# Optimization experiments

Hardware: AMD Instinct MI355X
Metric: run time of the kernel (lower is better)

## Reference

```python
import math
import jax, jax.numpy as jnp
import numpy as np

B, V, F, H, W = 1, 2, 4, 16, 28
TPF = H * W            # 448 tokens per frame
VS = F * TPF           # 1792 tokens per view
TS = V * VS            # 3584 total tokens
DIM, NH = 1536, 12
HD = DIM // NH         # 128
EPS = 1e-6
SCALE = 1.0 / math.sqrt(HD)


def _rope_angle_table(max_len=1024):
    # Wan-style 3D rope: head_dim//2 = 64 channels split [22, 21, 21] for (f, h, w)
    parts = []
    for full in (44, 42, 42):
        inv = 1.0 / (10000.0 ** (np.arange(0, full, 2) / full))
        parts.append(np.outer(np.arange(max_len), inv))
    return np.concatenate(parts, axis=1).astype(np.float32)  # [max_len, 64]


def setup_inputs():
    key = jax.random.key(0)
    ks = jax.random.split(key, 6)
    p = lambda k, shp: 0.02 * jax.random.normal(k, shp, dtype=jnp.float32)
    return {
        "x": jax.random.normal(ks[0], (B, TS, DIM), dtype=jnp.float32),
        "freqs": jnp.asarray(_rope_angle_table()),
        "q_w": p(ks[1], (DIM, DIM)), "q_b": jnp.zeros((DIM,), jnp.float32),
        "k_w": p(ks[2], (DIM, DIM)), "k_b": jnp.zeros((DIM,), jnp.float32),
        "v_w": p(ks[3], (DIM, DIM)), "v_b": jnp.zeros((DIM,), jnp.float32),
        "o_w": p(ks[4], (DIM, DIM)), "o_b": jnp.zeros((DIM,), jnp.float32),
        "norm_q_w": jnp.ones((DIM,), jnp.float32),
        "norm_k_w": jnp.ones((DIM,), jnp.float32),
        "seq_lens": jnp.full((B,), TS, jnp.int32),
        "view_grid_sizes": jnp.broadcast_to(jnp.array([F, H, W], jnp.int32), (B, V, 3)),
        "view_seq_lens": jnp.full((B, V), VS, jnp.int32),
        "total_seq_lens": jnp.full((B,), TS, jnp.int32),
    }


def _rms_norm(x, w):
    x32 = x.astype(jnp.float32)
    y = x32 * jax.lax.rsqrt(jnp.mean(x32 * x32, axis=-1, keepdims=True) + EPS)
    return y.astype(x.dtype) * w


def _rope_angles(freqs):
    c = HD // 2                                   # 64
    s0, s1 = c - 2 * (c // 3), c // 3             # 22, 21
    af = jnp.broadcast_to(freqs[:F, None, None, :s0], (F, H, W, s0))
    ah = jnp.broadcast_to(freqs[None, :H, None, s0:s0 + s1], (F, H, W, s1))
    aw = jnp.broadcast_to(freqs[None, None, :W, s0 + s1:c], (F, H, W, c - s0 - s1))
    return jnp.concatenate([af, ah, aw], axis=-1).reshape(VS, c)  # [VS, 64]


def _apply_rope(x, ang):
    # x: [N, S, NH, HD]; pairs are (x[..., 2i], x[..., 2i+1]) as in view_as_complex
    cos = jnp.cos(ang)[None, :, None, :]
    sin = jnp.sin(ang)[None, :, None, :]
    xr = x.reshape(x.shape[:-1] + (HD // 2, 2))
    r0 = xr[..., 0] * cos - xr[..., 1] * sin
    r1 = xr[..., 0] * sin + xr[..., 1] * cos
    return jnp.stack([r0, r1], axis=-1).reshape(x.shape)


def _attn_lse(q, k, v):
    # q,k,v: [N, S, NH, HD] -> out [N, S, NH, HD], lse [N, S, NH]
    logits = jnp.einsum('bqhd,bkhd->bhqk', q, k) * SCALE
    lse = jax.nn.logsumexp(logits, axis=-1)       # [N, NH, Sq]
    p = jnp.exp(logits - lse[..., None])
    out = jnp.einsum('bhqk,bkhd->bqhd', p, v)
    return out, jnp.transpose(lse, (0, 2, 1))


def _forward(x, freqs, q_w, q_b, k_w, k_b, v_w, v_b, o_w, o_b, norm_q_w, norm_k_w):
    xv = x[:, :TS]
    q = _rms_norm(xv @ q_w.T + q_b, norm_q_w)
    k = _rms_norm(xv @ k_w.T + k_b, norm_k_w)
    v = xv @ v_w.T + v_b
    q = q.reshape(B * V, VS, NH, HD)
    k = k.reshape(B * V, VS, NH, HD)
    v = v.reshape(B * V, VS, NH, HD)
    ang = _rope_angles(freqs)
    q = _apply_rope(q, ang)
    k = _apply_rope(k, ang)
    # intra-view attention over the full view sequence
    out_i, lse_i = _attn_lse(q, k, v)
    # cross-view per-frame attention: swap the two views for K/V
    k_sw = k.reshape(B, V, F, TPF, NH, HD)[:, ::-1].reshape(B * V * F, TPF, NH, HD)
    v_sw = v.reshape(B, V, F, TPF, NH, HD)[:, ::-1].reshape(B * V * F, TPF, NH, HD)
    q_c = q.reshape(B * V * F, TPF, NH, HD)
    out_c, lse_c = _attn_lse(q_c, k_sw, v_sw)
    out_i = out_i.reshape(B, V, F, TPF, NH, HD)
    lse_i = lse_i.reshape(B, V, F, TPF, NH)
    out_c = out_c.reshape(B, V, F, TPF, NH, HD)
    lse_c = lse_c.reshape(B, V, F, TPF, NH)
    # online-softmax-style LSE merge of the two attention results
    lse_u = jnp.logaddexp(lse_i, lse_c)
    fused = (jnp.exp(lse_i - lse_u)[..., None] * out_i
             + jnp.exp(lse_c - lse_u)[..., None] * out_c)
    fused = fused.reshape(B, TS, DIM)
    return fused @ o_w.T + o_b


def reference(x, freqs, q_w, q_b, k_w, k_b, v_w, v_b, o_w, o_b, norm_q_w, norm_k_w,
              seq_lens, view_grid_sizes, view_seq_lens, total_seq_lens):
    del seq_lens, view_grid_sizes, view_seq_lens, total_seq_lens  # validated layout constants
    return _forward(x, freqs, q_w, q_b, k_w, k_b, v_w, v_b, o_w, o_b, norm_q_w, norm_k_w)
```

## Files before the change

kernel.cpp:

```cpp
#include <hip/hip_runtime.h>

#define TS 3584
#define VS 1792
#define TPF 448
#define NHEAD 12
#define HDIM 128
#define DMODEL 1536
#define QK_PRESCALE (0.08838834764831845f * 1.4426950408889634f)

typedef unsigned short u16;
typedef unsigned int u32;
typedef __attribute__((ext_vector_type(8))) short bf16x8;
typedef __attribute__((ext_vector_type(4))) float f32x4;

__device__ __forceinline__ float u2f(u32 u) { union { u32 u; float f; } c; c.u = u; return c.f; }
__device__ __forceinline__ float blo(u32 u) { return u2f(u << 16); }
__device__ __forceinline__ float bhi(u32 u) { return u2f(u & 0xffff0000u); }
__device__ __forceinline__ u16 f2b(float f) {
  union { float f; u32 u; } c; c.f = f;
  return (u16)((c.u + 0x7fffu + ((c.u >> 16) & 1u)) >> 16);
}

__device__ __forceinline__ void gl16(const u16* g, u16* l) {
  __builtin_amdgcn_global_load_lds(
      (const __attribute__((address_space(1))) void*)g,
      (__attribute__((address_space(3))) void*)l, 16, 0, 0);
}

__global__ __launch_bounds__(256) void convert_bf16(
    const float* __restrict__ x, const float* __restrict__ qw,
    const float* __restrict__ kw, const float* __restrict__ vw,
    const float* __restrict__ ow, u16* __restrict__ xb,
    u16* __restrict__ wqkv, u16* __restrict__ owb) {
  const int z = blockIdx.y;
  const float* src;
  u16* dst;
  int n8;
  if (z == 0)      { src = x;  dst = xb;  n8 = TS * DMODEL / 8; }
  else if (z == 4) { src = ow; dst = owb; n8 = DMODEL * DMODEL / 8; }
  else {
    src = (z == 1) ? qw : (z == 2) ? kw : vw;
    dst = wqkv + (size_t)(z - 1) * DMODEL * DMODEL;
    n8 = DMODEL * DMODEL / 8;
  }
  const int idx = blockIdx.x * 256 + threadIdx.x;
  if (idx >= n8) return;
  const float4 a = ((const float4*)src)[2 * idx];
  const float4 b = ((const float4*)src)[2 * idx + 1];
  uint4 o;
  o.x = (u32)f2b(a.x) | ((u32)f2b(a.y) << 16);
  o.y = (u32)f2b(a.z) | ((u32)f2b(a.w) << 16);
  o.z = (u32)f2b(b.x) | ((u32)f2b(b.y) << 16);
  o.w = (u32)f2b(b.z) | ((u32)f2b(b.w) << 16);
  ((uint4*)dst)[idx] = o;
}

template <bool QKV>
__global__ __launch_bounds__(256) void gemm_mfma(
    const u16* __restrict__ A, const u16* __restrict__ W,
    const float* __restrict__ b0, const float* __restrict__ b1,
    const float* __restrict__ b2,
    u16* __restrict__ o0, u16* __restrict__ o1, u16* __restrict__ o2,
    float* __restrict__ of) {
  __shared__ __align__(16) u16 Als[128 * 64];
  __shared__ __align__(16) u16 Bls[128 * 64];
  const int t = threadIdx.x;
  const int wave = t >> 6, lane = t & 63, col = lane & 15, quad = lane >> 4;
  const int m0 = blockIdx.y * 128, n0 = blockIdx.x * 128;
  const int wm = (wave & 1) * 64, wn = (wave >> 1) * 64;
  f32x4 acc[4][4];
#pragma unroll
  for (int i = 0; i < 4; ++i)
#pragma unroll
    for (int j = 0; j < 4; ++j) acc[i][j] = (f32x4){0.f, 0.f, 0.f, 0.f};

  for (int k0 = 0; k0 < DMODEL; k0 += 64) {
    __syncthreads();
#pragma unroll
    for (int i = 0; i < 4; ++i) {
      const int idx = t + i * 256;
      const int row = idx >> 3, ch = idx & 7;
      *(uint4*)&Als[row * 64 + ((ch ^ (row & 7)) * 8)] =
          *(const uint4*)(A + (size_t)(m0 + row) * DMODEL + k0 + ch * 8);
      *(uint4*)&Bls[row * 64 + ((ch ^ (row & 7)) * 8)] =
          *(const uint4*)(W + (size_t)(n0 + row) * DMODEL + k0 + ch * 8);
    }
    __syncthreads();
#pragma unroll
    for (int s = 0; s < 2; ++s) {
      bf16x8 af[4], bv[4];
#pragma unroll
      for (int i = 0; i < 4; ++i) {
        const int r = wm + i * 16 + col;
        af[i] = *(const bf16x8*)&Als[r * 64 + (((s * 4 + quad) ^ (r & 7)) * 8)];
      }
#pragma unroll
      for (int j = 0; j < 4; ++j) {
        const int r = wn + j * 16 + col;
        bv[j] = *(const bf16x8*)&Bls[r * 64 + (((s * 4 + quad) ^ (r & 7)) * 8)];
      }
#pragma unroll
      for (int i = 0; i < 4; ++i)
#pragma unroll
        for (int j = 0; j < 4; ++j)
          acc[i][j] = __builtin_amdgcn_mfma_f32_16x16x32_bf16(af[i], bv[j], acc[i][j], 0, 0, 0);
    }
  }

#pragma unroll
  for (int j = 0; j < 4; ++j) {
    const int ng = n0 + wn + j * 16 + col;
    if constexpr (QKV) {
      const int sec = ng / DMODEL;
      const int nn = ng - sec * DMODEL;
      u16* dst = sec == 0 ? o0 : (sec == 1 ? o1 : o2);
      const float bias = sec == 0 ? b0[nn] : (sec == 1 ? b1[nn] : b2[nn]);
#pragma unroll
      for (int i = 0; i < 4; ++i) {
        const int mb = m0 + wm + i * 16 + quad * 4;
#pragma unroll
        for (int r = 0; r < 4; ++r)
          dst[(size_t)(mb + r) * DMODEL + nn] = f2b(acc[i][j][r] + bias);
      }
    } else {
      const float bias = b0[ng];
#pragma unroll
      for (int i = 0; i < 4; ++i) {
        const int mb = m0 + wm + i * 16 + quad * 4;
#pragma unroll
        for (int r = 0; r < 4; ++r)
          of[(size_t)(mb + r) * DMODEL + ng] = acc[i][j][r] + bias;
      }
    }
  }
}

__global__ __launch_bounds__(256) void rmsnorm_rope(
    u16* qbuf, u16* kbuf, const float* __restrict__ freqs,
    const float* __restrict__ nqw, const float* __restrict__ nkw) {
  const int tok = blockIdx.x;
  u32* row = (u32*)((blockIdx.y == 0 ? qbuf : kbuf) + (size_t)tok * DMODEL);
  const float* w = blockIdx.y == 0 ? nqw : nkw;
  const int t = threadIdx.x;
  const u32 u0 = row[t], u1 = row[t + 256], u2 = row[t + 512];
  float px[3] = { blo(u0), blo(u1), blo(u2) };
  float py[3] = { bhi(u0), bhi(u1), bhi(u2) };
  float ss = px[0] * px[0] + py[0] * py[0] + px[1] * px[1] + py[1] * py[1] +
             px[2] * px[2] + py[2] * py[2];
#pragma unroll
  for (int off = 32; off; off >>= 1) ss += __shfl_xor(ss, off);
  __shared__ float red[4];
  if ((t & 63) == 0) red[t >> 6] = ss;
  __syncthreads();
  float rstd = rsqrtf((red[0] + red[1] + red[2] + red[3]) * (1.0f / DMODEL) + 1e-6f);
  if (blockIdx.y == 0) rstd *= QK_PRESCALE;
  const int p = tok % VS;
  const int fi = p / TPF, rem = p % TPF, hi = rem / 28, wi = rem % 28;
#pragma unroll
  for (int jj = 0; jj < 3; ++jj) {
    const int pj = t + jj * 256;
    const int i = pj & 63;
    const int prow = (i < 22) ? fi : ((i < 43) ? hi : wi);
    const float ang = freqs[prow * 64 + i];
    float sn, cs;
    sincosf(ang, &sn, &cs);
    const float a = px[jj] * rstd * w[2 * pj], b = py[jj] * rstd * w[2 * pj + 1];
    row[pj] = (u32)f2b(a * cs - b * sn) | ((u32)f2b(a * sn + b * cs) << 16);
  }
}

__global__ __launch_bounds__(128) void transpose_v(
    const u16* __restrict__ v, u16* __restrict__ vt) {
  __shared__ __align__(16) u16 T[128 * 128];
  const int h = blockIdx.y;
  const int t0 = blockIdx.x * 128;
  const int t = threadIdx.x;
#pragma unroll
  for (int i = 0; i < 16; ++i) {
    int idx = t + i * 128;
    int tok = idx >> 4, hd8 = idx & 15;
    *(uint4*)&T[tok * 128 + ((hd8 ^ (tok & 7)) * 8)] =
        *(const uint4*)(v + (size_t)(t0 + tok) * DMODEL + h * HDIM + hd8 * 8);
  }
  __syncthreads();
  const int hb = t >> 3;
#pragma unroll
  for (int half = 0; half < 2; ++half) {
    const int tb = (t & 7) + half * 8;
    uint4 M[8];
#pragma unroll
    for (int r = 0; r < 8; ++r)
      M[r] = *(const uint4*)&T[(tb * 8 + r) * 128 + ((hb ^ r) * 8)];
    uint4 O[8];
#pragma unroll
    for (int c2 = 0; c2 < 4; ++c2) {
      const u32* A = (const u32*)&M[2 * c2];
      const u32* Bp = (const u32*)&M[2 * c2 + 1];
#pragma unroll
      for (int jh = 0; jh < 4; ++jh) {
        u32 a = A[jh], b = Bp[jh];
        ((u32*)&O[2 * jh])[c2] = (a & 0xffffu) | (b << 16);
        ((u32*)&O[2 * jh + 1])[c2] = (a >> 16) | (b & 0xffff0000u);
      }
    }
#pragma unroll
    for (int j = 0; j < 8; ++j)
      *(uint4*)(vt + (size_t)(h * HDIM + hb * 8 + j) * TS + t0 + tb * 8) = O[j];
  }
}

__global__ __launch_bounds__(256) void attn_mfma(
    const u16* __restrict__ q, const u16* __restrict__ k,
    const u16* __restrict__ vt, u16* __restrict__ fused) {
  __shared__ __align__(16) u16 Qls[64 * 128];
  __shared__ __align__(16) u16 Kls[2][32 * 128];
  __shared__ __align__(16) u16 Vls[2][128 * 32];
  const int t = threadIdx.x;
  const int wave = t >> 6, lane = t & 63;
  const int col = lane & 15, quad = lane >> 4;
  const int d = blockIdx.y * 56 + blockIdx.x;
  const int wk = (d & 7) * 84 + (d >> 3);
  const int h = wk / 56;
  const int qb = wk - h * 56;
  const int q0 = qb * 64;
  const int vview = q0 / VS;
  const int fidx = (q0 % VS) / TPF;
  const int base0 = vview * VS;
  const int base1 = (1 - vview) * VS + fidx * TPF;

#pragma unroll
  for (int j = 0; j < 4; ++j) {
    const int ci = (wave * 4 + j) * 64 + lane;
    const int qr = ci >> 4, c = ci & 15;
    gl16(q + (size_t)(q0 + qr) * DMODEL + h * HDIM + ((c ^ (qr & 7)) << 3),
         &Qls[(wave * 4 + j) * 512]);
  }
  const u16* ksrc[2];
  const u16* vsrc[2];
#pragma unroll
  for (int j = 0; j < 2; ++j) {
    const int ci = (wave * 2 + j) * 64 + lane;
    const int key = ci >> 4, c = ci & 15;
    const int k4 = ((key >> 1) & 12) | (key & 3);
    ksrc[j] = k + (size_t)key * DMODEL + h * HDIM + ((c ^ k4) << 3);
    const int hd = ci >> 2, s3 = ci & 3;
    vsrc[j] = vt + (size_t)(h * HDIM + hd) * TS + ((s3 ^ (hd & 3)) << 3);
  }
#pragma unroll
  for (int j = 0; j < 2; ++j) {
    gl16(ksrc[j] + (size_t)base0 * DMODEL, &Kls[0][(wave * 2 + j) * 512]);
    gl16(vsrc[j] + base0, &Vls[0][(wave * 2 + j) * 512]);
  }
  asm volatile("s_waitcnt vmcnt(4)" ::: "memory");
  __builtin_amdgcn_s_barrier();
  asm volatile("" ::: "memory");

  bf16x8 qfrag[4];
#pragma unroll
  for (int c = 0; c < 4; ++c)
    qfrag[c] = *(const bf16x8*)&Qls[(wave * 16 + col) * 128 +
                                    (((c * 4 + quad) ^ (col & 7)) << 3)];
  const int r0 = ((col & 12) << 1) | (col & 3);

  f32x4 accO[8];
#pragma unroll
  for (int c = 0; c < 8; ++c) accO[c] = (f32x4){0.f, 0.f, 0.f, 0.f};
  float m_run = -1e30f, l_run = 0.f;

  int cur = 0;
  for (int it = 0; it < 70; ++it) {
    if (it < 69) {
      const int it1 = it + 1;
      const int nb = (it1 < 56) ? base0 + it1 * 32 : base1 + (it1 - 56) * 32;
      const size_t ko = (size_t)nb * DMODEL;
#pragma unroll
      for (int j = 0; j < 2; ++j) {
        gl16(ksrc[j] + ko, &Kls[cur ^ 1][(wave * 2 + j) * 512]);
        gl16(vsrc[j] + nb, &Vls[cur ^ 1][(wave * 2 + j) * 512]);
      }
      asm volatile("s_waitcnt vmcnt(4)" ::: "memory");
    } else {
      asm volatile("s_waitcnt vmcnt(0)" ::: "memory");
    }
    __builtin_amdgcn_s_barrier();
    asm volatile("" ::: "memory");

    const u16* Kb = Kls[cur];
    const u16* Vb = Vls[cur];
    f32x4 s0 = (f32x4){0.f, 0.f, 0.f, 0.f}, s1 = (f32x4){0.f, 0.f, 0.f, 0.f};
    __builtin_amdgcn_s_setprio(1);
#pragma unroll
    for (int c = 0; c < 4; ++c) {
      const int x = ((c * 4 + quad) ^ col) << 3;
      bf16x8 ka0 = *(const bf16x8*)&Kb[r0 * 128 + x];
      bf16x8 ka1 = *(const bf16x8*)&Kb[(r0 + 4) * 128 + x];
      s0 = __builtin_amdgcn_mfma_f32_16x16x32_bf16(ka0, qfrag[c], s0, 0, 0, 0);
      s1 = __builtin_amdgcn_mfma_f32_16x16x32_bf16(ka1, qfrag[c], s1, 0, 0, 0);
    }
    __builtin_amdgcn_s_setprio(0);

    float lmax = fmaxf(fmaxf(fmaxf(s0[0], s0[1]), fmaxf(s0[2], s0[3])),
                       fmaxf(fmaxf(s1[0], s1[1]), fmaxf(s1[2], s1[3])));
    lmax = fmaxf(lmax, __shfl_xor(lmax, 16));
    lmax = fmaxf(lmax, __shfl_xor(lmax, 32));
    if (__any(lmax > m_run + 8.f)) {
      const float mnew = fmaxf(m_run, lmax);
      const float alpha = exp2f(m_run - mnew);
#pragma unroll
      for (int c = 0; c < 8; ++c) {
        accO[c][0] *= alpha; accO[c][1] *= alpha;
        accO[c][2] *= alpha; accO[c][3] *= alpha;
      }
      l_run *= alpha;
      m_run = mnew;
    }
    float p0[4], p1[4], ps = 0.f;
#pragma unroll
    for (int r = 0; r < 4; ++r) {
      p0[r] = exp2f(s0[r] - m_run);
      p1[r] = exp2f(s1[r] - m_run);
      ps += p0[r] + p1[r];
    }
    union { u32 w[4]; bf16x8 v; } pu;
    asm("v_cvt_pk_bf16_f32 %0, %1, %2" : "=v"(pu.w[0]) : "v"(p0[0]), "v"(p0[1]));
    asm("v_cvt_pk_bf16_f32 %0, %1, %2" : "=v"(pu.w[1]) : "v"(p0[2]), "v"(p0[3]));
    asm("v_cvt_pk_bf16_f32 %0, %1, %2" : "=v"(pu.w[2]) : "v"(p1[0]), "v"(p1[1]));
    asm("v_cvt_pk_bf16_f32 %0, %1, %2" : "=v"(pu.w[3]) : "v"(p1[2]), "v"(p1[3]));

    __builtin_amdgcn_s_setprio(1);
#pragma unroll
    for (int c = 0; c < 8; ++c) {
      bf16x8 va = *(const bf16x8*)&Vb[(c * 16 + col) * 32 + ((quad ^ (col & 3)) << 3)];
      accO[c] = __builtin_amdgcn_mfma_f32_16x16x32_bf16(va, pu.v, accO[c], 0, 0, 0);
    }
    __builtin_amdgcn_s_setprio(0);

    ps += __shfl_xor(ps, 16);
    ps += __shfl_xor(ps, 32);
    l_run += ps;

    asm volatile("" ::: "memory");
    __builtin_amdgcn_s_barrier();
    cur ^= 1;
  }

  const float inv = 1.0f / l_run;
  const int token = q0 + wave * 16 + col;
  u16* orow = fused + (size_t)token * DMODEL + h * HDIM;
#pragma unroll
  for (int c = 0; c < 8; ++c) {
    uint2 ov;
    ov.x = (u32)f2b(accO[c][0] * inv) | ((u32)f2b(accO[c][1] * inv) << 16);
    ov.y = (u32)f2b(accO[c][2] * inv) | ((u32)f2b(accO[c][3] * inv) << 16);
    *(uint2*)(orow + c * 16 + quad * 4) = ov;
  }
}

extern "C" void kernel_launch(void* const* d_in, const int* in_sizes, int n_in,
                              void* d_out, int out_size, void* d_ws, size_t ws_size,
                              hipStream_t stream) {
  (void)in_sizes; (void)n_in; (void)out_size; (void)ws_size;
  const float* x   = (const float*)d_in[0];
  const float* fr  = (const float*)d_in[1];
  const float* qw  = (const float*)d_in[2];
  const float* qb  = (const float*)d_in[3];
  const float* kw  = (const float*)d_in[4];
  const float* kb  = (const float*)d_in[5];
  const float* vw  = (const float*)d_in[6];
  const float* vb  = (const float*)d_in[7];
  const float* ow  = (const float*)d_in[8];
  const float* ob  = (const float*)d_in[9];
  const float* nqw = (const float*)d_in[10];
  const float* nkw = (const float*)d_in[11];

  u16* qf   = (u16*)d_ws;
  u16* vf   = qf + (size_t)TS * DMODEL;
  u16* xb   = vf + (size_t)TS * DMODEL;
  u16* wqkv = xb + (size_t)TS * DMODEL;
  u16* owb  = wqkv + (size_t)3 * DMODEL * DMODEL;
  u16* kf   = (u16*)d_out;
  u16* vtb  = (u16*)d_out + (size_t)TS * DMODEL;

  convert_bf16<<<dim3(TS * DMODEL / 8 / 256, 5), dim3(256), 0, stream>>>(
      x, qw, kw, vw, ow, xb, wqkv, owb);
  gemm_mfma<true><<<dim3(3 * DMODEL / 128, TS / 128), dim3(256), 0, stream>>>(
      xb, wqkv, qb, kb, vb, qf, kf, vf, nullptr);
  rmsnorm_rope<<<dim3(TS, 2), dim3(256), 0, stream>>>(qf, kf, fr, nqw, nkw);
  transpose_v<<<dim3(TS / 128, NHEAD), dim3(128), 0, stream>>>(vf, vtb);
  attn_mfma<<<dim3(TS / 64, NHEAD), dim3(256), 0, stream>>>(qf, kf, vtb, qf);
  gemm_mfma<false><<<dim3(DMODEL / 128, TS / 128), dim3(256), 0, stream>>>(
      qf, owb, ob, nullptr, nullptr, nullptr, nullptr, nullptr, (float*)d_out);
}
```

Measured before the change: 348.4 us.

## Widen attention KV tiles to 64 keys with split K/V prefetch pipeline

Restructures the attention inner loop to process 64 keys per iteration instead of 32, with K double-buffered and V single-buffered and issued early, so the V load overlaps the QK matmul and softmax. Q fragments are read directly from global memory instead of being staged through LDS, and exp2f is replaced with the hardware v_exp_f32 instruction. The loop is manually unrolled by two with compile-time buffer indices. The goal is fewer barriers per key and better overlap of memory with MFMA work, at the cost of more registers and an extra barrier between the S and PV phases.

```diff
diff --git a/kernel.cpp b/kernel.cpp
--- a/kernel.cpp
+++ b/kernel.cpp
@@ -19,6 +19,14 @@
 __device__ __forceinline__ u16 f2b(float f) {
   union { float f; u32 u; } c; c.f = f;
   return (u16)((c.u + 0x7fffu + ((c.u >> 16) & 1u)) >> 16);
+}
+
+__device__ __forceinline__ float exp2fast(float x) {
+#if __has_builtin(__builtin_amdgcn_exp2f)
+  return __builtin_amdgcn_exp2f(x);
+#else
+  float r; asm("v_exp_f32 %0, %1" : "=v"(r) : "v"(x)); return r;
+#endif
 }
 
 __device__ __forceinline__ void gl16(const u16* g, u16* l) {
@@ -212,9 +220,8 @@
 __global__ __launch_bounds__(256) void attn_mfma(
     const u16* __restrict__ q, const u16* __restrict__ k,
     const u16* __restrict__ vt, u16* __restrict__ fused) {
-  __shared__ __align__(16) u16 Qls[64 * 128];
-  __shared__ __align__(16) u16 Kls[2][32 * 128];
-  __shared__ __align__(16) u16 Vls[2][128 * 32];
+  __shared__ __align__(16) u16 Kls[2 * 64 * 128];
+  __shared__ __align__(16) u16 Vls[64 * 128];
   const int t = threadIdx.x;
   const int wave = t >> 6, lane = t & 63;
   const int col = lane & 15, quad = lane >> 4;
@@ -227,122 +234,140 @@
   const int fidx = (q0 % VS) / TPF;
   const int base0 = vview * VS;
   const int base1 = (1 - vview) * VS + fidx * TPF;
-
+  const int jmp = base1 - (base0 + 27 * 64);
+
+  bf16x8 qfrag[4];
+#pragma unroll
+  for (int c = 0; c < 4; ++c)
+    qfrag[c] = *(const bf16x8*)(q + (size_t)(q0 + wave * 16 + col) * DMODEL +
+                                h * HDIM + ((c * 4 + quad) << 3));
+
+  const u16* ksrc[4];
+  const u16* vsrc[4];
 #pragma unroll
   for (int j = 0; j < 4; ++j) {
     const int ci = (wave * 4 + j) * 64 + lane;
-    const int qr = ci >> 4, c = ci & 15;
-    gl16(q + (size_t)(q0 + qr) * DMODEL + h * HDIM + ((c ^ (qr & 7)) << 3),
-         &Qls[(wave * 4 + j) * 512]);
-  }
-  const u16* ksrc[2];
-  const u16* vsrc[2];
-#pragma unroll
-  for (int j = 0; j < 2; ++j) {
-    const int ci = (wave * 2 + j) * 64 + lane;
     const int key = ci >> 4, c = ci & 15;
-    const int k4 = ((key >> 1) & 12) | (key & 3);
-    ksrc[j] = k + (size_t)key * DMODEL + h * HDIM + ((c ^ k4) << 3);
-    const int hd = ci >> 2, s3 = ci & 3;
-    vsrc[j] = vt + (size_t)(h * HDIM + hd) * TS + ((s3 ^ (hd & 3)) << 3);
-  }
-#pragma unroll
-  for (int j = 0; j < 2; ++j) {
-    gl16(ksrc[j] + (size_t)base0 * DMODEL, &Kls[0][(wave * 2 + j) * 512]);
-    gl16(vsrc[j] + base0, &Vls[0][(wave * 2 + j) * 512]);
-  }
-  asm volatile("s_waitcnt vmcnt(4)" ::: "memory");
-  __builtin_amdgcn_s_barrier();
-  asm volatile("" ::: "memory");
-
-  bf16x8 qfrag[4];
-#pragma unroll
-  for (int c = 0; c < 4; ++c)
-    qfrag[c] = *(const bf16x8*)&Qls[(wave * 16 + col) * 128 +
-                                    (((c * 4 + quad) ^ (col & 7)) << 3)];
+    const int krow = key & 31;
+    const int k4 = ((krow >> 1) & 12) | (krow & 3);
+    ksrc[j] = k + (size_t)(base0 + key) * DMODEL + h * HDIM + ((c ^ k4) << 3);
+    const int sub = ci >> 9, hd = (ci >> 2) & 127, sl = ci & 3;
+    vsrc[j] = vt + (size_t)(h * HDIM + hd) * TS + base0 + sub * 32 +
+              ((sl ^ (hd & 3)) << 3);
+  }
   const int r0 = ((col & 12) << 1) | (col & 3);
+  int koffu[4];
+#pragma unroll
+  for (int c = 0; c < 4; ++c) koffu[c] = r0 * 128 + (((c * 4 + quad) ^ col) << 3);
+  const int voffu = col * 32 + ((quad ^ (col & 3)) << 3);
+
+#pragma unroll
+  for (int j = 0; j < 4; ++j)
+    gl16(ksrc[j], &Kls[(wave * 4 + j) * 512]);
+  int tK = 0, tV = 0;
+  {
+    const int dK = (tK == 27) ? jmp : 64; ++tK;
+#pragma unroll
+    for (int j = 0; j < 4; ++j) ksrc[j] += (ptrdiff_t)dK * DMODEL;
+  }
 
   f32x4 accO[8];
 #pragma unroll
   for (int c = 0; c < 8; ++c) accO[c] = (f32x4){0.f, 0.f, 0.f, 0.f};
   float m_run = -1e30f, l_run = 0.f;
 
-  int cur = 0;
-  for (int it = 0; it < 70; ++it) {
-    if (it < 69) {
-      const int it1 = it + 1;
-      const int nb = (it1 < 56) ? base0 + it1 * 32 : base1 + (it1 - 56) * 32;
-      const size_t ko = (size_t)nb * DMODEL;
-#pragma unroll
-      for (int j = 0; j < 2; ++j) {
-        gl16(ksrc[j] + ko, &Kls[cur ^ 1][(wave * 2 + j) * 512]);
-        gl16(vsrc[j] + nb, &Vls[cur ^ 1][(wave * 2 + j) * 512]);
-      }
-      asm volatile("s_waitcnt vmcnt(4)" ::: "memory");
-    } else {
-      asm volatile("s_waitcnt vmcnt(0)" ::: "memory");
-    }
-    __builtin_amdgcn_s_barrier();
-    asm volatile("" ::: "memory");
-
-    const u16* Kb = Kls[cur];
-    const u16* Vb = Vls[cur];
-    f32x4 s0 = (f32x4){0.f, 0.f, 0.f, 0.f}, s1 = (f32x4){0.f, 0.f, 0.f, 0.f};
-    __builtin_amdgcn_s_setprio(1);
-#pragma unroll
-    for (int c = 0; c < 4; ++c) {
-      const int x = ((c * 4 + quad) ^ col) << 3;
-      bf16x8 ka0 = *(const bf16x8*)&Kb[r0 * 128 + x];
-      bf16x8 ka1 = *(const bf16x8*)&Kb[(r0 + 4) * 128 + x];
-      s0 = __builtin_amdgcn_mfma_f32_16x16x32_bf16(ka0, qfrag[c], s0, 0, 0, 0);
-      s1 = __builtin_amdgcn_mfma_f32_16x16x32_bf16(ka1, qfrag[c], s1, 0, 0, 0);
-    }
-    __builtin_amdgcn_s_setprio(0);
-
-    float lmax = fmaxf(fmaxf(fmaxf(s0[0], s0[1]), fmaxf(s0[2], s0[3])),
-                       fmaxf(fmaxf(s1[0], s1[1]), fmaxf(s1[2], s1[3])));
-    lmax = fmaxf(lmax, __shfl_xor(lmax, 16));
-    lmax = fmaxf(lmax, __shfl_xor(lmax, 32));
-    if (__any(lmax > m_run + 8.f)) {
-      const float mnew = fmaxf(m_run, lmax);
-      const float alpha = exp2f(m_run - mnew);
-#pragma unroll
-      for (int c = 0; c < 8; ++c) {
-        accO[c][0] *= alpha; accO[c][1] *= alpha;
-        accO[c][2] *= alpha; accO[c][3] *= alpha;
-      }
-      l_run *= alpha;
-      m_run = mnew;
-    }
-    float p0[4], p1[4], ps = 0.f;
-#pragma unroll
-    for (int r = 0; r < 4; ++r) {
-      p0[r] = exp2f(s0[r] - m_run);
-      p1[r] = exp2f(s1[r] - m_run);
-      ps += p0[r] + p1[r];
-    }
-    union { u32 w[4]; bf16x8 v; } pu;
-    asm("v_cvt_pk_bf16_f32 %0, %1, %2" : "=v"(pu.w[0]) : "v"(p0[0]), "v"(p0[1]));
-    asm("v_cvt_pk_bf16_f32 %0, %1, %2" : "=v"(pu.w[1]) : "v"(p0[2]), "v"(p0[3]));
-    asm("v_cvt_pk_bf16_f32 %0, %1, %2" : "=v"(pu.w[2]) : "v"(p1[0]), "v"(p1[1]));
-    asm("v_cvt_pk_bf16_f32 %0, %1, %2" : "=v"(pu.w[3]) : "v"(p1[2]), "v"(p1[3]));
-
-    __builtin_amdgcn_s_setprio(1);
-#pragma unroll
-    for (int c = 0; c < 8; ++c) {
-      bf16x8 va = *(const bf16x8*)&Vb[(c * 16 + col) * 32 + ((quad ^ (col & 3)) << 3)];
-      accO[c] = __builtin_amdgcn_mfma_f32_16x16x32_bf16(va, pu.v, accO[c], 0, 0, 0);
-    }
-    __builtin_amdgcn_s_setprio(0);
-
-    ps += __shfl_xor(ps, 16);
-    ps += __shfl_xor(ps, 32);
-    l_run += ps;
-
-    asm volatile("" ::: "memory");
-    __builtin_amdgcn_s_barrier();
-    cur ^= 1;
-  }
+#define AITER(CUR, LAST)                                                       \
+  do {                                                                         \
+    _Pragma("unroll") for (int j = 0; j < 4; ++j)                              \
+        gl16(vsrc[j], &Vls[(wave * 4 + j) * 512]);                             \
+    {                                                                          \
+      const int dV = (tV == 27) ? jmp : 64; ++tV;                              \
+      _Pragma("unroll") for (int j = 0; j < 4; ++j) vsrc[j] += (ptrdiff_t)dV;  \
+    }                                                                          \
+    if (!(LAST)) {                                                             \
+      _Pragma("unroll") for (int j = 0; j < 4; ++j)                            \
+          gl16(ksrc[j], &Kls[((CUR) ^ 1) * 8192 + (wave * 4 + j) * 512]);      \
+      const int dK = (tK == 27) ? jmp : 64; ++tK;                              \
+      _Pragma("unroll") for (int j = 0; j < 4; ++j)                            \
+          ksrc[j] += (ptrdiff_t)dK * DMODEL;                                   \
+    }                                                                          \
+    asm volatile("s_waitcnt vmcnt(%0)" ::"i"((LAST) ? 4 : 8) : "memory");      \
+    __builtin_amdgcn_s_barrier();                                              \
+    asm volatile("" ::: "memory");                                             \
+    f32x4 s0 = (f32x4){0.f, 0.f, 0.f, 0.f}, s1 = s0, s2 = s0, s3 = s0;        \
+    __builtin_amdgcn_s_setprio(1);                                             \
+    _Pragma("unroll") for (int c = 0; c < 4; ++c) {                            \
+      bf16x8 ka0 = *(const bf16x8*)&Kls[(CUR)*8192 + koffu[c]];                \
+      bf16x8 ka1 = *(const bf16x8*)&Kls[(CUR)*8192 + koffu[c] + 512];          \
+      s0 = __builtin_amdgcn_mfma_f32_16x16x32_bf16(ka0, qfrag[c], s0, 0, 0, 0);\
+      s1 = __builtin_amdgcn_mfma_f32_16x16x32_bf16(ka1, qfrag[c], s1, 0, 0, 0);\
+    }                                                                          \
+    _Pragma("unroll") for (int c = 0; c < 4; ++c) {                            \
+      bf16x8 kb0 = *(const bf16x8*)&Kls[(CUR)*8192 + 4096 + koffu[c]];         \
+      bf16x8 kb1 = *(const bf16x8*)&Kls[(CUR)*8192 + 4096 + koffu[c] + 512];   \
+      s2 = __builtin_amdgcn_mfma_f32_16x16x32_bf16(kb0, qfrag[c], s2, 0, 0, 0);\
+      s3 = __builtin_amdgcn_mfma_f32_16x16x32_bf16(kb1, qfrag[c], s3, 0, 0, 0);\
+    }                                                                          \
+    __builtin_amdgcn_s_setprio(0);                                             \
+    float lmax = fmaxf(fmaxf(fmaxf(s0[0], s0[1]), fmaxf(s0[2], s0[3])),        \
+                       fmaxf(fmaxf(s1[0], s1[1]), fmaxf(s1[2], s1[3])));       \
+    lmax = fmaxf(lmax, fmaxf(fmaxf(fmaxf(s2[0], s2[1]), fmaxf(s2[2], s2[3])),  \
+                             fmaxf(fmaxf(s3[0], s3[1]), fmaxf(s3[2], s3[3]))));\
+    lmax = fmaxf(lmax, __shfl_xor(lmax, 16));                                  \
+    lmax = fmaxf(lmax, __shfl_xor(lmax, 32));                                  \
+    if (__any(lmax > m_run + 8.f)) {                                           \
+      const float mnew = fmaxf(m_run, lmax);                                   \
+      const float alpha = exp2fast(m_run - mnew);                              \
+      _Pragma("unroll") for (int c = 0; c < 8; ++c) {                          \
+        accO[c][0] *= alpha; accO[c][1] *= alpha;                              \
+        accO[c][2] *= alpha; accO[c][3] *= alpha;                              \
+      }                                                                        \
+      l_run *= alpha;                                                          \
+      m_run = mnew;                                                            \
+    }                                                                          \
+    float ps = 0.f;                                                            \
+    _Pragma("unroll") for (int r = 0; r < 4; ++r) {                            \
+      s0[r] = exp2fast(s0[r] - m_run); s1[r] = exp2fast(s1[r] - m_run);        \
+      s2[r] = exp2fast(s2[r] - m_run); s3[r] = exp2fast(s3[r] - m_run);        \
+      ps += (s0[r] + s1[r]) + (s2[r] + s3[r]);                                 \
+    }                                                                          \
+    union { u32 w[4]; bf16x8 v; } pu0, pu1;                                    \
+    asm("v_cvt_pk_bf16_f32 %0, %1, %2" : "=v"(pu0.w[0]) : "v"(s0[0]), "v"(s0[1])); \
+    asm("v_cvt_pk_bf16_f32 %0, %1, %2" : "=v"(pu0.w[1]) : "v"(s0[2]), "v"(s0[3])); \
+    asm("v_cvt_pk_bf16_f32 %0, %1, %2" : "=v"(pu0.w[2]) : "v"(s1[0]), "v"(s1[1])); \
+    asm("v_cvt_pk_bf16_f32 %0, %1, %2" : "=v"(pu0.w[3]) : "v"(s1[2]), "v"(s1[3])); \
+    asm("v_cvt_pk_bf16_f32 %0, %1, %2" : "=v"(pu1.w[0]) : "v"(s2[0]), "v"(s2[1])); \
+    asm("v_cvt_pk_bf16_f32 %0, %1, %2" : "=v"(pu1.w[1]) : "v"(s2[2]), "v"(s2[3])); \
+    asm("v_cvt_pk_bf16_f32 %0, %1, %2" : "=v"(pu1.w[2]) : "v"(s3[0]), "v"(s3[1])); \
+    asm("v_cvt_pk_bf16_f32 %0, %1, %2" : "=v"(pu1.w[3]) : "v"(s3[2]), "v"(s3[3])); \
+    asm volatile("s_waitcnt vmcnt(%0)" ::"i"((LAST) ? 0 : 4) : "memory");      \
+    __builtin_amdgcn_s_barrier();                                              \
+    asm volatile("" ::: "memory");                                             \
+    __builtin_amdgcn_s_setprio(1);                                             \
+    _Pragma("unroll") for (int c = 0; c < 8; ++c) {                            \
+      bf16x8 va0 = *(const bf16x8*)&Vls[voffu + c * 512];                      \
+      accO[c] = __builtin_amdgcn_mfma_f32_16x16x32_bf16(va0, pu0.v, accO[c], 0, 0, 0); \
+    }                                                                          \
+    _Pragma("unroll") for (int c = 0; c < 8; ++c) {                            \
+      bf16x8 va1 = *(const bf16x8*)&Vls[4096 + voffu + c * 512];               \
+      accO[c] = __builtin_amdgcn_mfma_f32_16x16x32_bf16(va1, pu1.v, accO[c], 0, 0, 0); \
+    }                                                                          \
+    __builtin_amdgcn_s_setprio(0);                                             \
+    ps += __shfl_xor(ps, 16);                                                  \
+    ps += __shfl_xor(ps, 32);                                                  \
+    l_run += ps;                                                               \
+    if (!(LAST)) {                                                             \
+      asm volatile("" ::: "memory");                                           \
+      __builtin_amdgcn_s_barrier();                                            \
+    }                                                                          \
+  } while (0)
+
+  for (int tt = 0; tt < 17; ++tt) {
+    AITER(0, false);
+    AITER(1, false);
+  }
+  AITER(0, true);
+#undef AITER
 
   const float inv = 1.0f / l_run;
   const int token = q0 + wave * 16 + col;
```

Result: slower. 360.2 us (+3.4%).
